# Performance work log

Hardware: AMD Instinct MI355X
Metric: run time of the kernel (lower is better)

Reference implementation:

```python
import jax, jax.numpy as jnp
import numpy as np

N_NODES = 100000
N_EDGES = 800000
IN_DIM, HID_DIM, OUT_DIM = 256, 128, 64


def setup_inputs() -> dict:
    key = jax.random.key(0)
    k1, k2, k3, k4 = jax.random.split(key, 4)
    x = jax.random.normal(k1, (N_NODES, IN_DIM), dtype=jnp.float32)
    edge_index = jax.random.randint(k2, (2, N_EDGES), 0, N_NODES, dtype=jnp.int64)
    # Glorot-style init scaled params
    W1 = jax.random.normal(k3, (IN_DIM, HID_DIM), dtype=jnp.float32) * (1.0 / np.sqrt(IN_DIM))
    b1 = jnp.zeros((HID_DIM,), dtype=jnp.float32)
    W2 = jax.random.normal(k4, (HID_DIM, OUT_DIM), dtype=jnp.float32) * (1.0 / np.sqrt(HID_DIM))
    b2 = jnp.zeros((OUT_DIM,), dtype=jnp.float32)
    return {"x": x, "edge_index": edge_index, "W1": W1, "b1": b1, "W2": W2, "b2": b2}


def reference(x, edge_index, W1, b1, W2, b2):
    n = x.shape[0]
    # GCNConv default: add self-loops, symmetric normalization D^-1/2 (A+I) D^-1/2
    loop = jnp.arange(n, dtype=edge_index.dtype)
    src = jnp.concatenate([edge_index[0], loop])
    dst = jnp.concatenate([edge_index[1], loop])
    deg = jax.ops.segment_sum(jnp.ones(src.shape, dtype=x.dtype), dst, num_segments=n)
    dinv = jax.lax.rsqrt(deg)  # deg >= 1 thanks to self-loops
    norm = dinv[src] * dinv[dst]  # [E+N]

    def gcn_conv(h, W, b):
        hw = h @ W                                         # [N, d_out] dense transform first (d_out < d_in)
        msg = hw[src] * norm[:, None]                      # gather + scale, [E+N, d_out]
        agg = jax.ops.segment_sum(msg, dst, num_segments=n)
        return agg + b

    h = jax.nn.relu(gcn_conv(x, W1, b1))
    return gcn_conv(h, W2, b2)
```

## Files before the change

kernel.cpp:

```cpp
#include <hip/hip_runtime.h>

typedef unsigned int uint;
typedef unsigned short ushort;
typedef __attribute__((ext_vector_type(8))) short bf16x8;
typedef __attribute__((ext_vector_type(4))) float f32x4;

#define NN 100000
#define NE 800000
#define D_IN 256
#define D_HID 128
#define D_OUT 64

__device__ __forceinline__ ushort f2bf(float f) {
    uint u = __float_as_uint(f);
    return (ushort)((u + 0x7fffu + ((u >> 16) & 1u)) >> 16);
}
__device__ __forceinline__ float bflo(uint u) { return __uint_as_float(u << 16); }
__device__ __forceinline__ float bfhi(uint u) { return __uint_as_float(u & 0xffff0000u); }
__device__ __forceinline__ uint pack2(float lo, float hi) {
    return (uint)f2bf(lo) | ((uint)f2bf(hi) << 16);
}
__device__ __forceinline__ bf16x8 pack8(float4 a, float4 b) {
    bf16x8 r;
    r[0] = (short)f2bf(a.x); r[1] = (short)f2bf(a.y); r[2] = (short)f2bf(a.z); r[3] = (short)f2bf(a.w);
    r[4] = (short)f2bf(b.x); r[5] = (short)f2bf(b.y); r[6] = (short)f2bf(b.z); r[7] = (short)f2bf(b.w);
    return r;
}

__global__ __launch_bounds__(256) void k_count(const int* __restrict__ dst, int* __restrict__ count, int e) {
    int i = blockIdx.x * 256 + threadIdx.x;
    if (i < e) {
        unsigned d = (unsigned)dst[i];
        if (d < NN) atomicAdd(&count[d], 1);
    }
}

#define SCAN_B 1024
__global__ __launch_bounds__(SCAN_B) void k_scan1(const int* __restrict__ count, int* __restrict__ incl,
                                                  int* __restrict__ blocksum, int n) {
    __shared__ int tmp[SCAN_B];
    int t = threadIdx.x;
    int gid = blockIdx.x * SCAN_B + t;
    int v = (gid < n) ? count[gid] : 0;
    tmp[t] = v;
    __syncthreads();
    for (int off = 1; off < SCAN_B; off <<= 1) {
        int u = (t >= off) ? tmp[t - off] : 0;
        __syncthreads();
        tmp[t] += u;
        __syncthreads();
    }
    if (gid < n) incl[gid] = tmp[t];
    if (t == SCAN_B - 1) blocksum[blockIdx.x] = tmp[t];
}

__global__ __launch_bounds__(256) void k_scan3(const int* __restrict__ incl, const int* __restrict__ count,
                                               const int* __restrict__ blocksum, int nb, int* __restrict__ offsets,
                                               int* __restrict__ cursor, float* __restrict__ dinv, int n) {
    __shared__ int bs[128];
    int t = threadIdx.x;
    if (t < 128) bs[t] = (t < nb) ? blocksum[t] : 0;
    __syncthreads();
    int i = blockIdx.x * 256 + t;
    if (i < n) {
        int b = i >> 10;
        int off = 0;
        for (int j = 0; j < b; j++) off += bs[j];
        int inc = incl[i] + off;
        int exc = inc - count[i];
        offsets[i] = exc;
        cursor[i] = exc;
        dinv[i] = rsqrtf((float)(count[i] + 1));
        if (i == n - 1) offsets[n] = inc;
    }
}

__global__ __launch_bounds__(256) void k_scatter(const int* __restrict__ edges, int* __restrict__ cursor,
                                                 int* __restrict__ srcs, int e) {
    int i = blockIdx.x * 256 + threadIdx.x;
    if (i < e) {
        unsigned s = (unsigned)edges[i];
        unsigned d = (unsigned)edges[e + i];
        if (s < NN && d < NN) {
            int pos = atomicAdd(&cursor[d], 1);
            srcs[pos] = (int)s;
        }
    }
}

__global__ __launch_bounds__(256) void k_castW(const float* __restrict__ W1, const float* __restrict__ W2,
                                               ushort* __restrict__ w1t, ushort* __restrict__ w2t) {
    int t = blockIdx.x * 256 + threadIdx.x;
    if (t < D_IN * D_HID) {
        int n = t / D_IN, k = t % D_IN;
        w1t[t] = f2bf(W1[(size_t)k * D_HID + n]);
    } else {
        int u = t - D_IN * D_HID;
        if (u < D_HID * D_OUT) {
            int n = u / D_HID, k = u % D_HID;
            w2t[u] = f2bf(W2[(size_t)k * D_OUT + n]);
        }
    }
}

template <int K_DIM, int N_DIM, bool AF32>
__global__ __launch_bounds__(256) void k_gemm16(const void* __restrict__ Av, const ushort* __restrict__ BT,
                                                const float* __restrict__ dinv, ushort* __restrict__ C, int M) {
    constexpr int NF = N_DIM / 16;
    constexpr int KK = K_DIM / 32;
    const int tid = threadIdx.x;
    const int w = tid >> 6, lane = tid & 63;
    const int l15 = lane & 15, g = lane >> 4;
    const int row0 = blockIdx.x * 64 + w * 16;
    const int row = min(row0 + l15, M - 1);

    bf16x8 a[KK];
    if constexpr (AF32) {
        const float* A = (const float*)Av;
        float4 ar[2 * KK];
#pragma unroll
        for (int kk = 0; kk < KK; kk++) {
            const float4* p = (const float4*)(A + (size_t)row * K_DIM + g * 8 + kk * 32);
            ar[2 * kk] = p[0];
            ar[2 * kk + 1] = p[1];
        }
#pragma unroll
        for (int kk = 0; kk < KK; kk++) a[kk] = pack8(ar[2 * kk], ar[2 * kk + 1]);
    } else {
        const ushort* A = (const ushort*)Av;
#pragma unroll
        for (int kk = 0; kk < KK; kk++)
            a[kk] = *reinterpret_cast<const bf16x8*>(A + (size_t)row * K_DIM + g * 8 + kk * 32);
    }

    f32x4 acc[NF];
#pragma unroll
    for (int nf = 0; nf < NF; nf++) acc[nf] = (f32x4){0.f, 0.f, 0.f, 0.f};

    const ushort* pb = BT + (size_t)l15 * K_DIM + g * 8;
#pragma unroll
    for (int kk = 0; kk < KK; kk++) {
#pragma unroll
        for (int nf = 0; nf < NF; nf++) {
            bf16x8 b = *reinterpret_cast<const bf16x8*>(pb + (size_t)nf * 16 * K_DIM + kk * 32);
            acc[nf] = __builtin_amdgcn_mfma_f32_16x16x32_bf16(a[kk], b, acc[nf], 0, 0, 0);
        }
    }

#pragma unroll
    for (int r = 0; r < 4; r++) {
        int rr = row0 + g * 4 + r;
        if (rr < M) {
            float dv = dinv[rr];
#pragma unroll
            for (int nf = 0; nf < NF; nf++)
                C[(size_t)rr * N_DIM + nf * 16 + l15] = f2bf(acc[nf][r] * dv);
        }
    }
}

__global__ __launch_bounds__(256) void k_agg128(const ushort* __restrict__ hws, const int* __restrict__ srcs,
                                                const int* __restrict__ offs, const float* __restrict__ dinv,
                                                const float* __restrict__ bias, ushort* __restrict__ outb, int n) {
    const int wv = threadIdx.x >> 6, lane = threadIdx.x & 63;
    const int node = blockIdx.x * 4 + wv;
    if (node >= n) return;
    const int g = lane >> 4, l15 = lane & 15;
    const int beg = offs[node];
    const int T = offs[node + 1] - beg + 1;
    const uint4* base = (const uint4*)hws;
    float acc[8] = {};
    int t = g;
    for (; t + 4 < T; t += 8) {
        int s0 = (t == 0) ? node : srcs[beg + t - 1];
        int s1 = srcs[beg + t + 3];
        uint4 va = base[(size_t)s0 * 16 + l15];
        uint4 vb = base[(size_t)s1 * 16 + l15];
        acc[0] += bflo(va.x) + bflo(vb.x); acc[1] += bfhi(va.x) + bfhi(vb.x);
        acc[2] += bflo(va.y) + bflo(vb.y); acc[3] += bfhi(va.y) + bfhi(vb.y);
        acc[4] += bflo(va.z) + bflo(vb.z); acc[5] += bfhi(va.z) + bfhi(vb.z);
        acc[6] += bflo(va.w) + bflo(vb.w); acc[7] += bfhi(va.w) + bfhi(vb.w);
    }
    for (; t < T; t += 4) {
        int s0 = (t == 0) ? node : srcs[beg + t - 1];
        uint4 va = base[(size_t)s0 * 16 + l15];
        acc[0] += bflo(va.x); acc[1] += bfhi(va.x);
        acc[2] += bflo(va.y); acc[3] += bfhi(va.y);
        acc[4] += bflo(va.z); acc[5] += bfhi(va.z);
        acc[6] += bflo(va.w); acc[7] += bfhi(va.w);
    }
#pragma unroll
    for (int j = 0; j < 8; j++) {
        acc[j] += __shfl_xor(acc[j], 16);
        acc[j] += __shfl_xor(acc[j], 32);
    }
    if (g == 0) {
        const float dv = dinv[node];
        const float4* b4 = (const float4*)(bias + 8 * l15);
        float4 bb0 = b4[0], bb1 = b4[1];
        uint4 o;
        o.x = pack2(fmaxf(acc[0] * dv + bb0.x, 0.f), fmaxf(acc[1] * dv + bb0.y, 0.f));
        o.y = pack2(fmaxf(acc[2] * dv + bb0.z, 0.f), fmaxf(acc[3] * dv + bb0.w, 0.f));
        o.z = pack2(fmaxf(acc[4] * dv + bb1.x, 0.f), fmaxf(acc[5] * dv + bb1.y, 0.f));
        o.w = pack2(fmaxf(acc[6] * dv + bb1.z, 0.f), fmaxf(acc[7] * dv + bb1.w, 0.f));
        ((uint4*)outb)[(size_t)node * 16 + l15] = o;
    }
}

__global__ __launch_bounds__(256) void k_agg64(const ushort* __restrict__ hws, const int* __restrict__ srcs,
                                               const int* __restrict__ offs, const float* __restrict__ dinv,
                                               const float* __restrict__ bias, float* __restrict__ out, int n) {
    const int wv = threadIdx.x >> 6, lane = threadIdx.x & 63;
    const int node = blockIdx.x * 4 + wv;
    if (node >= n) return;
    const int g = lane >> 3, l7 = lane & 7;
    const int beg = offs[node];
    const int T = offs[node + 1] - beg + 1;
    const uint4* base = (const uint4*)hws;
    float acc[8] = {};
    int t = g;
    for (; t + 8 < T; t += 16) {
        int s0 = (t == 0) ? node : srcs[beg + t - 1];
        int s1 = srcs[beg + t + 7];
        uint4 va = base[(size_t)s0 * 8 + l7];
        uint4 vb = base[(size_t)s1 * 8 + l7];
        acc[0] += bflo(va.x) + bflo(vb.x); acc[1] += bfhi(va.x) + bfhi(vb.x);
        acc[2] += bflo(va.y) + bflo(vb.y); acc[3] += bfhi(va.y) + bfhi(vb.y);
        acc[4] += bflo(va.z) + bflo(vb.z); acc[5] += bfhi(va.z) + bfhi(vb.z);
        acc[6] += bflo(va.w) + bflo(vb.w); acc[7] += bfhi(va.w) + bfhi(vb.w);
    }
    for (; t < T; t += 8) {
        int s0 = (t == 0) ? node : srcs[beg + t - 1];
        uint4 va = base[(size_t)s0 * 8 + l7];
        acc[0] += bflo(va.x); acc[1] += bfhi(va.x);
        acc[2] += bflo(va.y); acc[3] += bfhi(va.y);
        acc[4] += bflo(va.z); acc[5] += bfhi(va.z);
        acc[6] += bflo(va.w); acc[7] += bfhi(va.w);
    }
#pragma unroll
    for (int j = 0; j < 8; j++) {
        acc[j] += __shfl_xor(acc[j], 8);
        acc[j] += __shfl_xor(acc[j], 16);
        acc[j] += __shfl_xor(acc[j], 32);
    }
    if (g == 0) {
        const float dv = dinv[node];
        const float4* b4 = (const float4*)(bias + 8 * l7);
        float4 bb0 = b4[0], bb1 = b4[1];
        float4 o0, o1;
        o0.x = acc[0] * dv + bb0.x; o0.y = acc[1] * dv + bb0.y;
        o0.z = acc[2] * dv + bb0.z; o0.w = acc[3] * dv + bb0.w;
        o1.x = acc[4] * dv + bb1.x; o1.y = acc[5] * dv + bb1.y;
        o1.z = acc[6] * dv + bb1.z; o1.w = acc[7] * dv + bb1.w;
        ((float4*)out)[(size_t)node * 16 + 2 * l7] = o0;
        ((float4*)out)[(size_t)node * 16 + 2 * l7 + 1] = o1;
    }
}

static inline size_t align_up(size_t x, size_t a) { return (x + a - 1) & ~(a - 1); }

extern "C" void kernel_launch(void* const* d_in, const int* in_sizes, int n_in,
                              void* d_out, int out_size, void* d_ws, size_t ws_size,
                              hipStream_t stream) {
    const float* x = (const float*)d_in[0];
    const int* edges = (const int*)d_in[1];
    const float* W1 = (const float*)d_in[2];
    const float* b1 = (const float*)d_in[3];
    const float* W2 = (const float*)d_in[4];
    const float* b2 = (const float*)d_in[5];
    float* out = (float*)d_out;

    char* p = (char*)d_ws;
    int* count = (int*)p;      p += align_up(NN * 4, 256);
    int* incl = (int*)p;       p += align_up(NN * 4, 256);
    int* offsets = (int*)p;    p += align_up((NN + 1) * 4, 256);
    int* cursor = (int*)p;     p += align_up(NN * 4, 256);
    int* srcs = (int*)p;       p += align_up(NE * 4, 256);
    int* blocksum = (int*)p;   p += align_up(256 * 4, 256);
    float* dinv = (float*)p;   p += align_up(NN * 4, 256);
    ushort* w1t = (ushort*)p;  p += align_up(D_IN * D_HID * 2, 256);
    ushort* w2t = (ushort*)p;  p += align_up(D_HID * D_OUT * 2, 256);
    ushort* hw1s = (ushort*)p; p += align_up((size_t)NN * D_HID * 2, 256);
    ushort* hb = (ushort*)p;   p += align_up((size_t)NN * D_HID * 2, 256);
    ushort* hw2s = (ushort*)p; p += align_up((size_t)NN * D_OUT * 2, 256);

    const int nb_scan = (NN + SCAN_B - 1) / SCAN_B;

    hipMemsetAsync(count, 0, NN * 4, stream);
    k_count<<<(NE + 255) / 256, 256, 0, stream>>>(edges + NE, count, NE);
    k_scan1<<<nb_scan, SCAN_B, 0, stream>>>(count, incl, blocksum, NN);
    k_scan3<<<(NN + 255) / 256, 256, 0, stream>>>(incl, count, blocksum, nb_scan, offsets, cursor, dinv, NN);
    k_scatter<<<(NE + 255) / 256, 256, 0, stream>>>(edges, cursor, srcs, NE);
    k_castW<<<(D_IN * D_HID + D_HID * D_OUT + 255) / 256, 256, 0, stream>>>(W1, W2, w1t, w2t);

    const int g16_blocks = (NN + 63) / 64;

    k_gemm16<D_IN, D_HID, true><<<g16_blocks, 256, 0, stream>>>(x, w1t, dinv, hw1s, NN);
    k_agg128<<<(NN + 3) / 4, 256, 0, stream>>>(hw1s, srcs, offsets, dinv, b1, hb, NN);

    k_gemm16<D_HID, D_OUT, false><<<g16_blocks, 256, 0, stream>>>(hb, w2t, dinv, hw2s, NN);
    k_agg64<<<(NN + 3) / 4, 256, 0, stream>>>(hw2s, srcs, offsets, dinv, b2, out, NN);
}
```

Measured before the change: 410.1 us.

## Stage GEMM A tiles into LDS via async loads and split N across waves

Replaces the per-wave register GEMM with a block-level kernel that copies the A row tile into shared memory using global_load_lds with an XOR swizzle. Each wave then keeps its own slice of B columns in registers across several 16-row M tiles. Previously every wave loaded all of B for its own 16 rows. The aim is to cut redundant B traffic and get better coalesced A loads, at the cost of more LDS per block and possibly lower occupancy. The hb buffer is padded because the clamped row loads may read past the end.

```diff
diff --git a/kernel.cpp b/kernel.cpp
--- a/kernel.cpp
+++ b/kernel.cpp
@@ -103,58 +103,87 @@
     }
 }
 
-template <int K_DIM, int N_DIM, bool AF32>
-__global__ __launch_bounds__(256) void k_gemm16(const void* __restrict__ Av, const ushort* __restrict__ BT,
-                                                const float* __restrict__ dinv, ushort* __restrict__ C, int M) {
-    constexpr int NF = N_DIM / 16;
+template <int K_DIM, int N_DIM, bool AF32, int MT>
+__global__ __launch_bounds__(256) void k_gemm_stage(const void* __restrict__ Av, const ushort* __restrict__ BT,
+                                                    const float* __restrict__ dinv, ushort* __restrict__ C, int M) {
+    constexpr int NFW = N_DIM / 64;
     constexpr int KK = K_DIM / 32;
+    constexpr int BR = MT * 16;
+    constexpr int RB = K_DIM * (AF32 ? 4 : 2);
+    constexpr int LDSB = BR * RB;
+    constexpr int CH = LDSB / 16;
+    __shared__ char lds[LDSB];
+
     const int tid = threadIdx.x;
     const int w = tid >> 6, lane = tid & 63;
     const int l15 = lane & 15, g = lane >> 4;
-    const int row0 = blockIdx.x * 64 + w * 16;
-    const int row = min(row0 + l15, M - 1);
-
-    bf16x8 a[KK];
-    if constexpr (AF32) {
-        const float* A = (const float*)Av;
-        float4 ar[2 * KK];
-#pragma unroll
-        for (int kk = 0; kk < KK; kk++) {
-            const float4* p = (const float4*)(A + (size_t)row * K_DIM + g * 8 + kk * 32);
-            ar[2 * kk] = p[0];
-            ar[2 * kk + 1] = p[1];
-        }
-#pragma unroll
-        for (int kk = 0; kk < KK; kk++) a[kk] = pack8(ar[2 * kk], ar[2 * kk + 1]);
-    } else {
-        const ushort* A = (const ushort*)Av;
+    const int row0 = blockIdx.x * BR;
+    const int cb = w * 16 * NFW;
+
+    bf16x8 bf[NFW][KK];
+#pragma unroll
+    for (int nf = 0; nf < NFW; nf++)
 #pragma unroll
         for (int kk = 0; kk < KK; kk++)
-            a[kk] = *reinterpret_cast<const bf16x8*>(A + (size_t)row * K_DIM + g * 8 + kk * 32);
-    }
-
-    f32x4 acc[NF];
-#pragma unroll
-    for (int nf = 0; nf < NF; nf++) acc[nf] = (f32x4){0.f, 0.f, 0.f, 0.f};
-
-    const ushort* pb = BT + (size_t)l15 * K_DIM + g * 8;
+            bf[nf][kk] = *reinterpret_cast<const bf16x8*>(
+                BT + (size_t)(cb + nf * 16 + l15) * K_DIM + kk * 32 + g * 8);
+
+    {
+        const char* Ab = (const char*)Av;
+#pragma unroll
+        for (int i = 0; i < CH / 256; i++) {
+            int c = (i * 4 + w) * 64 + lane;
+            int p = c * 16;
+            int r = p / RB;
+            int off = p & (RB - 1);
+            int f = (r & 7) << 4;
+            int grow = min(row0 + r, M - 1);
+            const char* src = Ab + (size_t)grow * RB + (off ^ f);
+            __builtin_amdgcn_global_load_lds((const __attribute__((address_space(1))) void*)src,
+                                             (__attribute__((address_space(3))) void*)(lds + p), 16, 0, 0);
+        }
+    }
+    __syncthreads();
+
+    f32x4 acc[MT][NFW];
+#pragma unroll
+    for (int mt = 0; mt < MT; mt++)
+#pragma unroll
+        for (int nf = 0; nf < NFW; nf++) acc[mt][nf] = (f32x4){0.f, 0.f, 0.f, 0.f};
+
 #pragma unroll
     for (int kk = 0; kk < KK; kk++) {
 #pragma unroll
-        for (int nf = 0; nf < NF; nf++) {
-            bf16x8 b = *reinterpret_cast<const bf16x8*>(pb + (size_t)nf * 16 * K_DIM + kk * 32);
-            acc[nf] = __builtin_amdgcn_mfma_f32_16x16x32_bf16(a[kk], b, acc[nf], 0, 0, 0);
-        }
-    }
-
-#pragma unroll
-    for (int r = 0; r < 4; r++) {
-        int rr = row0 + g * 4 + r;
-        if (rr < M) {
-            float dv = dinv[rr];
-#pragma unroll
-            for (int nf = 0; nf < NF; nf++)
-                C[(size_t)rr * N_DIM + nf * 16 + l15] = f2bf(acc[nf][r] * dv);
+        for (int mt = 0; mt < MT; mt++) {
+            const int r = mt * 16 + l15;
+            const int f = (r & 7) << 4;
+            bf16x8 a;
+            if constexpr (AF32) {
+                const int o = kk * 128 + g * 32;
+                float4 v0 = *(const float4*)(lds + r * RB + (o ^ f));
+                float4 v1 = *(const float4*)(lds + r * RB + ((o + 16) ^ f));
+                a = pack8(v0, v1);
+            } else {
+                const int o = kk * 64 + g * 16;
+                a = *(const bf16x8*)(lds + r * RB + (o ^ f));
+            }
+#pragma unroll
+            for (int nf = 0; nf < NFW; nf++)
+                acc[mt][nf] = __builtin_amdgcn_mfma_f32_16x16x32_bf16(a, bf[nf][kk], acc[mt][nf], 0, 0, 0);
+        }
+    }
+
+#pragma unroll
+    for (int mt = 0; mt < MT; mt++) {
+#pragma unroll
+        for (int r4 = 0; r4 < 4; r4++) {
+            int rr = row0 + mt * 16 + g * 4 + r4;
+            if (rr < M) {
+                float dv = dinv[rr];
+#pragma unroll
+                for (int nf = 0; nf < NFW; nf++)
+                    C[(size_t)rr * N_DIM + cb + nf * 16 + l15] = f2bf(acc[mt][nf][r4] * dv);
+            }
         }
     }
 }
@@ -281,7 +310,7 @@
     ushort* w1t = (ushort*)p;  p += align_up(D_IN * D_HID * 2, 256);
     ushort* w2t = (ushort*)p;  p += align_up(D_HID * D_OUT * 2, 256);
     ushort* hw1s = (ushort*)p; p += align_up((size_t)NN * D_HID * 2, 256);
-    ushort* hb = (ushort*)p;   p += align_up((size_t)NN * D_HID * 2, 256);
+    ushort* hb = (ushort*)p;   p += align_up((size_t)NN * D_HID * 2 + 32 * 1024, 256);
     ushort* hw2s = (ushort*)p; p += align_up((size_t)NN * D_OUT * 2, 256);
 
     const int nb_scan = (NN + SCAN_B - 1) / SCAN_B;
@@ -293,11 +322,9 @@
     k_scatter<<<(NE + 255) / 256, 256, 0, stream>>>(edges, cursor, srcs, NE);
     k_castW<<<(D_IN * D_HID + D_HID * D_OUT + 255) / 256, 256, 0, stream>>>(W1, W2, w1t, w2t);
 
-    const int g16_blocks = (NN + 63) / 64;
-
-    k_gemm16<D_IN, D_HID, true><<<g16_blocks, 256, 0, stream>>>(x, w1t, dinv, hw1s, NN);
+    k_gemm_stage<D_IN, D_HID, true, 4><<<(NN + 63) / 64, 256, 0, stream>>>(x, w1t, dinv, hw1s, NN);
     k_agg128<<<(NN + 3) / 4, 256, 0, stream>>>(hw1s, srcs, offsets, dinv, b1, hb, NN);
 
-    k_gemm16<D_HID, D_OUT, false><<<g16_blocks, 256, 0, stream>>>(hb, w2t, dinv, hw2s, NN);
+    k_gemm_stage<D_HID, D_OUT, false, 8><<<(NN + 127) / 128, 256, 0, stream>>>(hb, w2t, dinv, hw2s, NN);
     k_agg64<<<(NN + 3) / 4, 256, 0, stream>>>(hw2s, srcs, offsets, dinv, b2, out, NN);
 }
```

After: 381.5 us. 1.08x faster.
